# Performance work log

Hardware: AMD Instinct MI355X
Metric: run time of the kernel (lower is better)

Reference implementation:

```python
import jax, jax.numpy as jnp
import numpy as np
import math

B, S, D_IN, D_ATTN, D_HID = 4, 2048, 1024, 1024, 1024

def gelu_erf(x):
    return 0.5 * x * (1.0 + jax.lax.erf(x / math.sqrt(2.0)))

def setup_inputs() -> dict:
    key = jax.random.key(0)
    k = jax.random.split(key, 8)
    inputs = jax.random.normal(k[0], (B, S, D_IN), dtype=jnp.float32)
    attn_mask = jax.random.randint(k[1], (B, S, S), 0, 2, dtype=jnp.int32)
    sq = 1.0 / math.sqrt(D_IN)
    Wq = jax.random.normal(k[2], (D_IN, D_ATTN), dtype=jnp.float32) * sq
    bq = jnp.zeros((D_ATTN,), dtype=jnp.float32)
    Wk = jax.random.normal(k[3], (D_IN, D_ATTN), dtype=jnp.float32) * sq
    bk = jnp.zeros((D_ATTN,), dtype=jnp.float32)
    Wv = jax.random.normal(k[4], (D_IN, D_HID), dtype=jnp.float32) * sq
    bv = jnp.zeros((D_HID,), dtype=jnp.float32)
    return {"inputs": inputs, "attn_mask": attn_mask,
            "Wq": Wq, "bq": bq, "Wk": Wk, "bk": bk, "Wv": Wv, "bv": bv}

def reference(inputs, attn_mask, Wq, bq, Wk, bk, Wv, bv):
    # Q, K: [B, S, d_k]
    Q = inputs @ Wq + bq
    K = inputs @ Wk + bk
    scores = jnp.einsum('bqd,bkd->bqk', Q, K) / math.sqrt(D_ATTN)
    scores = scores + attn_mask.astype(scores.dtype) * (-1e9)
    attn = jax.nn.softmax(scores, axis=-1)
    WV = gelu_erf(inputs @ Wv + bv)           # [B, S, hidden]
    context = jnp.einsum('bqk,bkh->bqh', attn, WV)
    return (context, attn)
```

## Files before the change

kernel.cpp:

```cpp
#include <hip/hip_runtime.h>
#include <hip/hip_bf16.h>
#include <math.h>

#define B_   4
#define S_   2048
#define DIN  1024
#define DATT 1024
#define DHID 1024

typedef short bf16x8 __attribute__((ext_vector_type(8)));
typedef float f32x4  __attribute__((ext_vector_type(4)));

__device__ inline unsigned short f2bf(float f) {
    unsigned u = __float_as_uint(f);
    u += 0x7fffu + ((u >> 16) & 1u);
    return (unsigned short)(u >> 16);
}
__device__ inline float bf2f(unsigned u16) {
    return __uint_as_float(u16 << 16);
}
__device__ inline void gld16(const void* g, void* l) {
    __builtin_amdgcn_global_load_lds(
        (const __attribute__((address_space(1))) unsigned int*)g,
        (__attribute__((address_space(3))) unsigned int*)l, 16, 0, 0);
}
__device__ inline void xswz(int& bx, int& by, int& bz)
{
    int gx = gridDim.x, gy = gridDim.y, gz = gridDim.z;
    int nwg = gx * gy * gz;
    int lin = blockIdx.x + gx * (blockIdx.y + gy * blockIdx.z);
    int swz = (nwg & 7) ? lin : ((lin & 7) * (nwg >> 3) + (lin >> 3));
    bx = swz % gx;
    int t = swz / gx;
    by = t % gy;
    bz = t / gy;
}

__global__ __launch_bounds__(256)
void xcvt_k(const float* __restrict__ x, unsigned short* __restrict__ xb)
{
    int i = blockIdx.x * 256 + threadIdx.x;
    const float4* p = (const float4*)x + (size_t)i * 2;
    float4 v0 = p[0], v1 = p[1];
    uint4 o;
    o.x = (unsigned)f2bf(v0.x) | ((unsigned)f2bf(v0.y) << 16);
    o.y = (unsigned)f2bf(v0.z) | ((unsigned)f2bf(v0.w) << 16);
    o.z = (unsigned)f2bf(v1.x) | ((unsigned)f2bf(v1.y) << 16);
    o.w = (unsigned)f2bf(v1.z) | ((unsigned)f2bf(v1.w) << 16);
    ((uint4*)xb)[i] = o;
}

__global__ __launch_bounds__(256)
void wcvt_k(const float* __restrict__ Wq, const float* __restrict__ Wk,
            const float* __restrict__ Wv, unsigned short* __restrict__ Wt)
{
    int w = blockIdx.y;
    const float* W = (w == 0) ? Wq : ((w == 1) ? Wk : Wv);
    unsigned short* D = Wt + (size_t)w * DIN * DATT;
    int t = blockIdx.x * 256 + threadIdx.x;
    int n  = t >> 6;
    int kc = (t & 63) * 16;
    unsigned short r[16];
#pragma unroll
    for (int i = 0; i < 16; ++i) r[i] = f2bf(W[(size_t)(kc + i) * DATT + n]);
    uint4 o0, o1;
    o0.x = (unsigned)r[0] | ((unsigned)r[1] << 16);  o0.y = (unsigned)r[2] | ((unsigned)r[3] << 16);
    o0.z = (unsigned)r[4] | ((unsigned)r[5] << 16);  o0.w = (unsigned)r[6] | ((unsigned)r[7] << 16);
    o1.x = (unsigned)r[8] | ((unsigned)r[9] << 16);  o1.y = (unsigned)r[10] | ((unsigned)r[11] << 16);
    o1.z = (unsigned)r[12] | ((unsigned)r[13] << 16); o1.w = (unsigned)r[14] | ((unsigned)r[15] << 16);
    *(uint4*)(D + (size_t)n * DIN + kc)     = o0;
    *(uint4*)(D + (size_t)n * DIN + kc + 8) = o1;
}

__global__ __launch_bounds__(256)
void mpack_k(const int* __restrict__ m, unsigned* __restrict__ mb)
{
    int w = blockIdx.x * 256 + threadIdx.x;
    const uint4* p = (const uint4*)(m + (size_t)w * 32);
    unsigned bits = 0;
#pragma unroll
    for (int g = 0; g < 8; ++g) {
        uint4 v = p[g];
        bits |= (v.x ? 1u : 0u) << (g * 4 + 0);
        bits |= (v.y ? 1u : 0u) << (g * 4 + 1);
        bits |= (v.z ? 1u : 0u) << (g * 4 + 2);
        bits |= (v.w ? 1u : 0u) << (g * 4 + 3);
    }
    mb[w] = bits;
}

template<int EPI>
__global__ __launch_bounds__(512, 4)
void gemmS_k(const unsigned short* __restrict__ Ap, const unsigned short* __restrict__ Bp,
             const float* __restrict__ b0, const float* __restrict__ b1,
             const float* __restrict__ b2, const unsigned* __restrict__ mbits,
             void* __restrict__ Cp, void* __restrict__ Cp2,
             int K, int lda, int ldb, int ldc,
             long aStride, long bStride, long cStride, float scale)
{
    __shared__ __align__(16) unsigned short Al[256][64];
    __shared__ __align__(16) unsigned short Bl[128][64];

    int bx, by, z;
    xswz(bx, by, z);
    const int tid  = threadIdx.x;
    const int row0 = by * 256;
    const int col0 = bx * 128;
    const int wid  = tid >> 6, lane = tid & 63;
    const int lr = lane & 15, lg = lane >> 4;
    const int wm = wid >> 1, wn = wid & 1;
    const int wb = (tid & 448) * 16;

    const unsigned short* Ab = Ap + (size_t)aStride * z;
    const unsigned short* Bb = Bp + (size_t)bStride * z;

    f32x4 acc[4][4] = {};
    const int nt = K >> 6;

    const int srow = tid >> 3, sj = tid & 7;

    for (int t = 0; t < nt; ++t) {
        const int k0 = t << 6;
#pragma unroll
        for (int r = 0; r < 4; ++r) {
            int row = r * 64 + srow;
            gld16(Ab + (size_t)(row0 + row) * lda + k0 + ((sj ^ (row & 7)) << 3),
                  (char*)&Al[0][0] + r * 8192 + wb);
        }
#pragma unroll
        for (int r = 0; r < 2; ++r) {
            int row = r * 64 + srow;
            gld16(Bb + (size_t)(col0 + row) * ldb + k0 + ((sj ^ (row & 7)) << 3),
                  (char*)&Bl[0][0] + r * 8192 + wb);
        }
        __syncthreads();
#pragma unroll
        for (int s = 0; s < 2; ++s) {
            bf16x8 av[4], bv[4];
#pragma unroll
            for (int i = 0; i < 4; ++i) {
                int ra = wm * 64 + i * 16 + lr;
                av[i] = *(const bf16x8*)((const char*)&Al[0][0] + ra * 128 + ((((s << 2) | lg) ^ (ra & 7)) << 4));
                int rb = wn * 64 + i * 16 + lr;
                bv[i] = *(const bf16x8*)((const char*)&Bl[0][0] + rb * 128 + ((((s << 2) | lg) ^ (rb & 7)) << 4));
            }
#pragma unroll
            for (int mi = 0; mi < 4; ++mi)
#pragma unroll
                for (int ni = 0; ni < 4; ++ni)
                    acc[mi][ni] = __builtin_amdgcn_mfma_f32_16x16x32_bf16(av[mi], bv[ni], acc[mi][ni], 0, 0, 0);
        }
        __syncthreads();
    }

    if (EPI == 6) {
        int w = col0 >> 10;
        int cb0 = (col0 & 1023) + wn * 64;
        if (w < 2) {
            unsigned short* C = (unsigned short*)Cp + (size_t)w * ((size_t)B_ * S_ * DATT);
            const float* bias = w ? b1 : b0;
#pragma unroll
            for (int ni = 0; ni < 4; ++ni) {
                int col = cb0 + ni * 16 + lr;
                float bb = bias[col];
#pragma unroll
                for (int mi = 0; mi < 4; ++mi) {
                    int rowb = row0 + wm * 64 + mi * 16 + lg * 4;
#pragma unroll
                    for (int v = 0; v < 4; ++v)
                        C[(size_t)(rowb + v) * DATT + col] = f2bf(acc[mi][ni][v] + bb);
                }
            }
        } else {
            unsigned short* C = (unsigned short*)Cp2;
            int zz = row0 >> 11;
            int sb = (row0 & 2047) + wm * 64;
#pragma unroll
            for (int ni = 0; ni < 4; ++ni) {
                int col = cb0 + ni * 16 + lr;
                float bb = b2[col];
#pragma unroll
                for (int mi = 0; mi < 4; ++mi) {
                    unsigned short r[4];
#pragma unroll
                    for (int v = 0; v < 4; ++v) {
                        float xv = acc[mi][ni][v] + bb;
                        xv = 0.5f * xv * (1.0f + erff(xv * 0.70710678118654752f));
                        r[v] = f2bf(xv);
                    }
                    uint2 o;
                    o.x = (unsigned)r[0] | ((unsigned)r[1] << 16);
                    o.y = (unsigned)r[2] | ((unsigned)r[3] << 16);
                    *(uint2*)(C + ((size_t)zz * DHID + col) * S_ + sb + mi * 16 + lg * 4) = o;
                }
            }
        }
    } else {
        unsigned short* C = (unsigned short*)Cp + (size_t)cStride * z;
        const unsigned* mb = mbits + (size_t)z * (S_ * S_ / 32);
        const int wbase = (col0 + wn * 64) >> 5;
#pragma unroll
        for (int mi = 0; mi < 4; ++mi) {
            int rowb = row0 + wm * 64 + mi * 16 + lg * 4;
#pragma unroll
            for (int v = 0; v < 4; ++v) {
                int row = rowb + v;
                unsigned w0 = mb[(size_t)row * (S_ / 32) + wbase];
                unsigned w1 = mb[(size_t)row * (S_ / 32) + wbase + 1];
#pragma unroll
                for (int ni = 0; ni < 4; ++ni) {
                    int col = col0 + wn * 64 + ni * 16 + lr;
                    unsigned wsel = (ni & 2) ? w1 : w0;
                    float ev = ((wsel >> ((ni & 1) * 16 + lr)) & 1)
                             ? 0.0f : __expf(acc[mi][ni][v] * scale);
                    C[(size_t)row * ldc + col] = f2bf(ev);
                }
            }
        }
    }
}

template<int AMODE, int EPI>
__global__ __launch_bounds__(256)
void gemm_k(const void* __restrict__ Ap, const unsigned short* __restrict__ Bp,
            const float* __restrict__ b0, const float* __restrict__ b1,
            const float* __restrict__ b2, const int* __restrict__ maskp,
            void* __restrict__ Cp, void* __restrict__ Cp2,
            int K, int lda, int ldb, int ldc,
            long aStride, long bStride, long cStride, long mStride, float scale)
{
    __shared__ __align__(16) unsigned short sh[2][2][128][64];
    int bx, by, z;
    xswz(bx, by, z);
    const int tid  = threadIdx.x;
    const int row0 = by * 128;
    const int col0 = bx * 128;
    const int wave = tid >> 6, lane = tid & 63;
    const int lr = lane & 15, lg = lane >> 4;
    const int wm = (wave >> 1) * 64, wn = (wave & 1) * 64;
    const unsigned short* Bb = Bp + (size_t)bStride * z;
    f32x4 acc[4][4] = {};
    const int nt = K >> 6;
    auto stage = [&](int b, int k0) {
        if (AMODE == 0) {
            const unsigned short* A = (const unsigned short*)Ap + (size_t)aStride * z;
#pragma unroll
            for (int q = 0; q < 4; ++q) {
                int c = q * 256 + tid;
                int row = c >> 3, j = c & 7;
                gld16((const char*)(A + (size_t)(row0 + row) * lda + k0) + ((j ^ (row & 7)) << 4),
                      (char*)&sh[b][0][0][0] + ((q * 256 + (tid & 192)) << 4));
            }
        } else {
            const float* A = (const float*)Ap + (size_t)aStride * z;
#pragma unroll
            for (int q = 0; q < 4; ++q) {
                int c = q * 256 + tid;
                int row = c >> 3, j = c & 7;
                const float* src = A + (size_t)(row0 + row) * lda + k0 + ((j ^ (row & 7)) << 3);
                float4 v0 = *(const float4*)src;
                float4 v1 = *(const float4*)(src + 4);
                uint4 p;
                p.x = (unsigned)f2bf(v0.x) | ((unsigned)f2bf(v0.y) << 16);
                p.y = (unsigned)f2bf(v0.z) | ((unsigned)f2bf(v0.w) << 16);
                p.z = (unsigned)f2bf(v1.x) | ((unsigned)f2bf(v1.y) << 16);
                p.w = (unsigned)f2bf(v1.z) | ((unsigned)f2bf(v1.w) << 16);
                *(uint4*)((char*)&sh[b][0][0][0] + ((size_t)c << 4)) = p;
            }
        }
#pragma unroll
        for (int q = 0; q < 4; ++q) {
            int c = q * 256 + tid;
            int row = c >> 3, j = c & 7;
            gld16((const char*)(Bb + (size_t)(col0 + row) * ldb + k0) + ((j ^ (row & 7)) << 4),
                  (char*)&sh[b][1][0][0] + ((q * 256 + (tid & 192)) << 4));
        }
    };
    stage(0, 0);
    __syncthreads();
    int cur = 0;
    for (int t = 0; t < nt; ++t) {
        if (t + 1 < nt) stage(cur ^ 1, (t + 1) << 6);
        const char* baseA = (const char*)&sh[cur][0][0][0];
        const char* baseB = (const char*)&sh[cur][1][0][0];
        bf16x8 af[2][4], bfv[2][4];
#pragma unroll
        for (int s = 0; s < 2; ++s)
#pragma unroll
            for (int i = 0; i < 4; ++i) {
                int ra = wm + i * 16 + lr;
                af[s][i]  = *(const bf16x8*)(baseA + ra * 128 + ((((s << 2) | lg) ^ (ra & 7)) << 4));
                int rb = wn + i * 16 + lr;
                bfv[s][i] = *(const bf16x8*)(baseB + rb * 128 + ((((s << 2) | lg) ^ (rb & 7)) << 4));
            }
#pragma unroll
        for (int s = 0; s < 2; ++s)
#pragma unroll
            for (int mi = 0; mi < 4; ++mi)
#pragma unroll
                for (int ni = 0; ni < 4; ++ni)
                    acc[mi][ni] = __builtin_amdgcn_mfma_f32_16x16x32_bf16(af[s][mi], bfv[s][ni], acc[mi][ni], 0, 0, 0);
        if (t + 1 < nt) __syncthreads();
        cur ^= 1;
    }
    if (EPI == 6) {
        int w = col0 >> 10;
        int cb = (col0 & 1023) + wn;
        if (w < 2) {
            unsigned short* C = (unsigned short*)Cp + (size_t)w * ((size_t)B_ * S_ * DATT);
            const float* bias = w ? b1 : b0;
#pragma unroll
            for (int mi = 0; mi < 4; ++mi)
#pragma unroll
                for (int ni = 0; ni < 4; ++ni) {
                    int col = cb + ni * 16 + lr;
                    float bb = bias[col];
                    int rowb = row0 + wm + mi * 16 + lg * 4;
#pragma unroll
                    for (int v = 0; v < 4; ++v)
                        C[(size_t)(rowb + v) * DATT + col] = f2bf(acc[mi][ni][v] + bb);
                }
        } else {
            unsigned short* C = (unsigned short*)Cp2;
            int zz = row0 >> 11;
            int sb = (row0 & 2047) + wm;
#pragma unroll
            for (int mi = 0; mi < 4; ++mi)
#pragma unroll
                for (int ni = 0; ni < 4; ++ni) {
                    int col = cb + ni * 16 + lr;
                    float bb = b2[col];
                    unsigned short r[4];
#pragma unroll
                    for (int v = 0; v < 4; ++v) {
                        float xv = acc[mi][ni][v] + bb;
                        xv = 0.5f * xv * (1.0f + erff(xv * 0.70710678118654752f));
                        r[v] = f2bf(xv);
                    }
                    uint2 o;
                    o.x = (unsigned)r[0] | ((unsigned)r[1] << 16);
                    o.y = (unsigned)r[2] | ((unsigned)r[3] << 16);
                    *(uint2*)(C + ((size_t)zz * DHID + col) * S_ + sb + mi * 16 + lg * 4) = o;
                }
        }
    } else if (EPI == 5) {
        float* C = (float*)Cp + (size_t)cStride * z;
        const float* invs = b0 + (size_t)z * S_;
#pragma unroll
        for (int mi = 0; mi < 4; ++mi)
#pragma unroll
            for (int ni = 0; ni < 4; ++ni) {
                int col = col0 + wn + ni * 16 + lr;
                int rowb = row0 + wm + mi * 16 + lg * 4;
#pragma unroll
                for (int v = 0; v < 4; ++v)
                    C[(size_t)(rowb + v) * ldc + col] = acc[mi][ni][v] * invs[rowb + v];
            }
    } else {
        float* C = (float*)Cp + (size_t)cStride * z;
        const int* mp = (EPI == 2) ? (maskp + (size_t)mStride * z) : nullptr;
#pragma unroll
        for (int mi = 0; mi < 4; ++mi)
#pragma unroll
            for (int ni = 0; ni < 4; ++ni) {
                int col = col0 + wn + ni * 16 + lr;
                int rowb = row0 + wm + mi * 16 + lg * 4;
#pragma unroll
                for (int v = 0; v < 4; ++v) {
                    float val = acc[mi][ni][v];
                    if (EPI == 2) val = val * scale + (float)mp[(size_t)(rowb + v) * ldc + col] * (-1e9f);
                    C[(size_t)(rowb + v) * ldc + col] = val;
                }
            }
    }
}

__global__ __launch_bounds__(256)
void rownormM_k(const unsigned short* __restrict__ e, float* __restrict__ attn,
                float* __restrict__ invs)
{
    const int row = blockIdx.x;
    const int tid = threadIdx.x;
    uint4 u = ((const uint4*)(e + (size_t)row * S_))[tid];
    float f[8];
    f[0] = bf2f(u.x & 0xffffu); f[1] = bf2f(u.x >> 16);
    f[2] = bf2f(u.y & 0xffffu); f[3] = bf2f(u.y >> 16);
    f[4] = bf2f(u.z & 0xffffu); f[5] = bf2f(u.z >> 16);
    f[6] = bf2f(u.w & 0xffffu); f[7] = bf2f(u.w >> 16);
    float s = ((f[0] + f[1]) + (f[2] + f[3])) + ((f[4] + f[5]) + (f[6] + f[7]));
#pragma unroll
    for (int o = 32; o; o >>= 1) s += __shfl_xor(s, o);
    __shared__ float red[4];
    if ((tid & 63) == 0) red[tid >> 6] = s;
    __syncthreads();
    s = (red[0] + red[1]) + (red[2] + red[3]);
    float inv = 1.0f / s;
    float* p = attn + (size_t)row * S_;
    ((float4*)p)[tid * 2]     = make_float4(f[0] * inv, f[1] * inv, f[2] * inv, f[3] * inv);
    ((float4*)p)[tid * 2 + 1] = make_float4(f[4] * inv, f[5] * inv, f[6] * inv, f[7] * inv);
    if (tid == 0) invs[row] = inv;
}

template<bool WRITEATTN>
__global__ __launch_bounds__(256)
void rownorm_k(const unsigned short* __restrict__ e, float* __restrict__ attn,
               float* __restrict__ invs)
{
    const int row = blockIdx.x;
    const int tid = threadIdx.x;
    uint4 u = ((const uint4*)(e + (size_t)row * S_))[tid];
    float f[8];
    f[0] = bf2f(u.x & 0xffffu); f[1] = bf2f(u.x >> 16);
    f[2] = bf2f(u.y & 0xffffu); f[3] = bf2f(u.y >> 16);
    f[4] = bf2f(u.z & 0xffffu); f[5] = bf2f(u.z >> 16);
    f[6] = bf2f(u.w & 0xffffu); f[7] = bf2f(u.w >> 16);
    float s = ((f[0] + f[1]) + (f[2] + f[3])) + ((f[4] + f[5]) + (f[6] + f[7]));
#pragma unroll
    for (int o = 32; o; o >>= 1) s += __shfl_xor(s, o);
    __shared__ float red[4];
    if ((tid & 63) == 0) red[tid >> 6] = s;
    __syncthreads();
    s = (red[0] + red[1]) + (red[2] + red[3]);
    float inv = 1.0f / s;
    if (WRITEATTN) {
        float* p = attn + (size_t)row * S_;
        ((float4*)p)[tid * 2]     = make_float4(f[0] * inv, f[1] * inv, f[2] * inv, f[3] * inv);
        ((float4*)p)[tid * 2 + 1] = make_float4(f[4] * inv, f[5] * inv, f[6] * inv, f[7] * inv);
    } else {
        if (tid == 0) invs[row] = inv;
    }
}

__global__ __launch_bounds__(256)
void softmax_k(float* __restrict__ attn)
{
    const int row = blockIdx.x;
    float* p = attn + (size_t)row * S_;
    const int tid = threadIdx.x;
    float4 a = ((const float4*)p)[tid * 2];
    float4 b = ((const float4*)p)[tid * 2 + 1];
    float m = fmaxf(fmaxf(fmaxf(a.x, a.y), fmaxf(a.z, a.w)),
                    fmaxf(fmaxf(b.x, b.y), fmaxf(b.z, b.w)));
#pragma unroll
    for (int o = 32; o; o >>= 1) m = fmaxf(m, __shfl_xor(m, o));
    __shared__ float redm[4];
    __shared__ float reds[4];
    if ((tid & 63) == 0) redm[tid >> 6] = m;
    __syncthreads();
    m = fmaxf(fmaxf(redm[0], redm[1]), fmaxf(redm[2], redm[3]));
    float e[8];
    e[0] = expf(a.x - m); e[1] = expf(a.y - m); e[2] = expf(a.z - m); e[3] = expf(a.w - m);
    e[4] = expf(b.x - m); e[5] = expf(b.y - m); e[6] = expf(b.z - m); e[7] = expf(b.w - m);
    float s = e[0] + e[1] + e[2] + e[3] + e[4] + e[5] + e[6] + e[7];
#pragma unroll
    for (int o = 32; o; o >>= 1) s += __shfl_xor(s, o);
    if ((tid & 63) == 0) reds[tid >> 6] = s;
    __syncthreads();
    s = reds[0] + reds[1] + reds[2] + reds[3];
    float inv = 1.0f / s;
    ((float4*)p)[tid * 2]     = make_float4(e[0] * inv, e[1] * inv, e[2] * inv, e[3] * inv);
    ((float4*)p)[tid * 2 + 1] = make_float4(e[4] * inv, e[5] * inv, e[6] * inv, e[7] * inv);
}

extern "C" void kernel_launch(void* const* d_in, const int* in_sizes, int n_in,
                              void* d_out, int out_size, void* d_ws, size_t ws_size,
                              hipStream_t stream)
{
    const float* x    = (const float*)d_in[0];
    const int*   mask = (const int*)d_in[1];
    const float* Wq   = (const float*)d_in[2];
    const float* bq   = (const float*)d_in[3];
    const float* Wk   = (const float*)d_in[4];
    const float* bk   = (const float*)d_in[5];
    const float* Wv   = (const float*)d_in[6];
    const float* bv   = (const float*)d_in[7];

    float* ctx  = (float*)d_out;
    float* attn = ctx + (size_t)B_ * S_ * DHID;

    unsigned short* Qb = (unsigned short*)ctx;
    unsigned short* Kb = Qb + (size_t)B_ * S_ * DATT;
    unsigned short* Xb = (unsigned short*)attn;
    unsigned short* Wb = Xb + (size_t)B_ * S_ * DIN;

    const size_t eElems  = (size_t)B_ * S_ * S_;
    const size_t mWords  = eElems / 32;
    const size_t wvElems = (size_t)B_ * DHID * S_;

    size_t needFast = eElems * 2 + (size_t)B_ * S_ * 4 + mWords * 4 + wvElems * 2 + 256;
    size_t needMid  = eElems * 2 + (size_t)B_ * S_ * 4 + mWords * 4 + 256;

    dim3 blk(256), blk5(512);

    xcvt_k<<<dim3(4096), blk, 0, stream>>>(x, Xb);
    wcvt_k<<<dim3(256, 3), blk, 0, stream>>>(Wq, Wk, Wv, Wb);

    if (ws_size >= needFast) {
        unsigned short* e    = (unsigned short*)d_ws;
        float*          invs = (float*)(e + eElems);
        unsigned*       mb   = (unsigned*)(invs + (size_t)B_ * S_);
        unsigned short* WVbT = (unsigned short*)(mb + mWords);

        mpack_k<<<dim3(mWords / 256), blk, 0, stream>>>(mask, mb);
        gemmS_k<6><<<dim3(24, 32, 1), blk5, 0, stream>>>(
            Xb, Wb, bq, bk, bv, nullptr, Qb, WVbT,
            DIN, DIN, DIN, 0, 0, 0, 0, 1.0f);
        gemmS_k<4><<<dim3(16, 8, 4), blk5, 0, stream>>>(
            Qb, Kb, nullptr, nullptr, nullptr, mb, e, nullptr,
            DATT, DATT, DATT, S_,
            (long)S_ * DATT, (long)S_ * DATT, (long)S_ * S_, 0.03125f);
        rownormM_k<<<dim3(B_ * S_), blk, 0, stream>>>(e, attn, invs);
        gemm_k<0, 5><<<dim3(8, 16, 4), blk, 0, stream>>>(
            e, WVbT, invs, nullptr, nullptr, nullptr, ctx, nullptr,
            S_, S_, S_, DHID,
            (long)S_ * S_, (long)DHID * S_, (long)S_ * DHID, 0, 1.0f);
    } else if (ws_size >= needMid) {
        unsigned short* e    = (unsigned short*)d_ws;
        float*          invs = (float*)(e + eElems);
        unsigned*       mb   = (unsigned*)(invs + (size_t)B_ * S_);
        unsigned short* WVbT = Wb + (size_t)3 * DIN * DATT;

        mpack_k<<<dim3(mWords / 256), blk, 0, stream>>>(mask, mb);
        gemmS_k<6><<<dim3(24, 32, 1), blk5, 0, stream>>>(
            Xb, Wb, bq, bk, bv, nullptr, Qb, WVbT,
            DIN, DIN, DIN, 0, 0, 0, 0, 1.0f);
        gemmS_k<4><<<dim3(16, 8, 4), blk5, 0, stream>>>(
            Qb, Kb, nullptr, nullptr, nullptr, mb, e, nullptr,
            DATT, DATT, DATT, S_,
            (long)S_ * DATT, (long)S_ * DATT, (long)S_ * S_, 0.03125f);
        rownorm_k<false><<<dim3(B_ * S_), blk, 0, stream>>>(e, nullptr, invs);
        gemm_k<0, 5><<<dim3(8, 16, 4), blk, 0, stream>>>(
            e, WVbT, invs, nullptr, nullptr, nullptr, ctx, nullptr,
            S_, S_, S_, DHID,
            (long)S_ * S_, (long)DHID * S_, (long)S_ * DHID, 0, 1.0f);
        rownorm_k<true><<<dim3(B_ * S_), blk, 0, stream>>>(e, attn, nullptr);
    } else {
        unsigned short* WVw = (unsigned short*)d_ws;
        gemm_k<0, 6><<<dim3(24, 64, 1), blk, 0, stream>>>(
            Xb, Wb, bq, bk, bv, nullptr, Qb, WVw,
            DIN, DIN, DIN, 0, 0, 0, 0, 0, 1.0f);
        gemm_k<0, 2><<<dim3(16, 16, 4), blk, 0, stream>>>(
            Qb, Kb, nullptr, nullptr, nullptr, mask, attn, nullptr,
            DATT, DATT, DATT, S_,
            (long)S_ * DATT, (long)S_ * DATT, (long)S_ * S_, (long)S_ * S_, 0.03125f);
        softmax_k<<<dim3(B_ * S_), blk, 0, stream>>>(attn);
        gemm_k<1, 3><<<dim3(8, 16, 4), blk, 0, stream>>>(
            attn, WVw, nullptr, nullptr, nullptr, nullptr, ctx, nullptr,
            S_, S_, S_, DHID,
            (long)S_ * S_, (long)DHID * S_, (long)S_ * DHID, 0, 1.0f);
    }
}
```

Measured before the change: 215.3 us.

## Stage GEMM epilogues through swizzled LDS, merge prep kernels, and tile block mapping

Merges the three preprocessing kernels (input convert, weight convert/transpose, mask bit-pack) into one launch to cut launch overhead. Changes the GEMM epilogues to write each warp's output tile into swizzled shared memory first, then issue 16-byte coalesced global stores instead of scattered 2-byte or 8-byte writes. Also remaps workgroup indices into 4x2 tiles so neighbouring blocks share A/B panels in cache. Costs some extra LDS traffic and wait instructions in the epilogue.

```diff
diff --git a/kernel.cpp b/kernel.cpp
--- a/kernel.cpp
+++ b/kernel.cpp
@@ -24,69 +24,79 @@
         (const __attribute__((address_space(1))) unsigned int*)g,
         (__attribute__((address_space(3))) unsigned int*)l, 16, 0, 0);
 }
-__device__ inline void xswz(int& bx, int& by, int& bz)
-{
-    int gx = gridDim.x, gy = gridDim.y, gz = gridDim.z;
-    int nwg = gx * gy * gz;
+
+__device__ inline void xmap(int& bx, int& by, int& z)
+{
+    int gx = gridDim.x, gy = gridDim.y;
+    int nwg = gx * gy * gridDim.z;
     int lin = blockIdx.x + gx * (blockIdx.y + gy * blockIdx.z);
-    int swz = (nwg & 7) ? lin : ((lin & 7) * (nwg >> 3) + (lin >> 3));
-    bx = swz % gx;
-    int t = swz / gx;
-    by = t % gy;
-    bz = t / gy;
+    int s = (nwg & 7) ? lin : ((lin & 7) * (nwg >> 3) + (lin >> 3));
+    if (!(gx & 3) && !(gy & 1)) {
+        int cpz = (gx >> 2) * (gy >> 1);
+        int chunk = s >> 3, w = s & 7;
+        int cz = chunk / cpz, c2 = chunk % cpz;
+        int cx = c2 % (gx >> 2), cy = c2 / (gx >> 2);
+        bx = cx * 4 + (w & 3);
+        by = cy * 2 + (w >> 2);
+        z  = cz;
+    } else {
+        bx = s % gx;
+        int t = s / gx;
+        by = t % gy;
+        z  = t / gy;
+    }
 }
 
 __global__ __launch_bounds__(256)
-void xcvt_k(const float* __restrict__ x, unsigned short* __restrict__ xb)
-{
-    int i = blockIdx.x * 256 + threadIdx.x;
-    const float4* p = (const float4*)x + (size_t)i * 2;
-    float4 v0 = p[0], v1 = p[1];
-    uint4 o;
-    o.x = (unsigned)f2bf(v0.x) | ((unsigned)f2bf(v0.y) << 16);
-    o.y = (unsigned)f2bf(v0.z) | ((unsigned)f2bf(v0.w) << 16);
-    o.z = (unsigned)f2bf(v1.x) | ((unsigned)f2bf(v1.y) << 16);
-    o.w = (unsigned)f2bf(v1.z) | ((unsigned)f2bf(v1.w) << 16);
-    ((uint4*)xb)[i] = o;
-}
-
-__global__ __launch_bounds__(256)
-void wcvt_k(const float* __restrict__ Wq, const float* __restrict__ Wk,
-            const float* __restrict__ Wv, unsigned short* __restrict__ Wt)
-{
-    int w = blockIdx.y;
-    const float* W = (w == 0) ? Wq : ((w == 1) ? Wk : Wv);
-    unsigned short* D = Wt + (size_t)w * DIN * DATT;
-    int t = blockIdx.x * 256 + threadIdx.x;
-    int n  = t >> 6;
-    int kc = (t & 63) * 16;
-    unsigned short r[16];
-#pragma unroll
-    for (int i = 0; i < 16; ++i) r[i] = f2bf(W[(size_t)(kc + i) * DATT + n]);
-    uint4 o0, o1;
-    o0.x = (unsigned)r[0] | ((unsigned)r[1] << 16);  o0.y = (unsigned)r[2] | ((unsigned)r[3] << 16);
-    o0.z = (unsigned)r[4] | ((unsigned)r[5] << 16);  o0.w = (unsigned)r[6] | ((unsigned)r[7] << 16);
-    o1.x = (unsigned)r[8] | ((unsigned)r[9] << 16);  o1.y = (unsigned)r[10] | ((unsigned)r[11] << 16);
-    o1.z = (unsigned)r[12] | ((unsigned)r[13] << 16); o1.w = (unsigned)r[14] | ((unsigned)r[15] << 16);
-    *(uint4*)(D + (size_t)n * DIN + kc)     = o0;
-    *(uint4*)(D + (size_t)n * DIN + kc + 8) = o1;
-}
-
-__global__ __launch_bounds__(256)
-void mpack_k(const int* __restrict__ m, unsigned* __restrict__ mb)
-{
-    int w = blockIdx.x * 256 + threadIdx.x;
-    const uint4* p = (const uint4*)(m + (size_t)w * 32);
-    unsigned bits = 0;
-#pragma unroll
-    for (int g = 0; g < 8; ++g) {
-        uint4 v = p[g];
-        bits |= (v.x ? 1u : 0u) << (g * 4 + 0);
-        bits |= (v.y ? 1u : 0u) << (g * 4 + 1);
-        bits |= (v.z ? 1u : 0u) << (g * 4 + 2);
-        bits |= (v.w ? 1u : 0u) << (g * 4 + 3);
-    }
-    mb[w] = bits;
+void prep_k(const float* __restrict__ x, unsigned short* __restrict__ xb,
+            const float* __restrict__ Wq, const float* __restrict__ Wk,
+            const float* __restrict__ Wv, unsigned short* __restrict__ Wt,
+            const int* __restrict__ m, unsigned* __restrict__ mb)
+{
+    const int b = blockIdx.x;
+    const int tid = threadIdx.x;
+    if (b < 4096) {
+        int i = b * 256 + tid;
+        const float4* p = (const float4*)x + (size_t)i * 2;
+        float4 v0 = p[0], v1 = p[1];
+        uint4 o;
+        o.x = (unsigned)f2bf(v0.x) | ((unsigned)f2bf(v0.y) << 16);
+        o.y = (unsigned)f2bf(v0.z) | ((unsigned)f2bf(v0.w) << 16);
+        o.z = (unsigned)f2bf(v1.x) | ((unsigned)f2bf(v1.y) << 16);
+        o.w = (unsigned)f2bf(v1.z) | ((unsigned)f2bf(v1.w) << 16);
+        ((uint4*)xb)[i] = o;
+    } else if (b < 4864) {
+        int idx = b - 4096;
+        int w = idx >> 8;
+        const float* W = (w == 0) ? Wq : ((w == 1) ? Wk : Wv);
+        unsigned short* D = Wt + (size_t)w * DIN * DATT;
+        int t = (idx & 255) * 256 + tid;
+        int n  = t >> 6;
+        int kc = (t & 63) * 16;
+        unsigned short r[16];
+#pragma unroll
+        for (int i = 0; i < 16; ++i) r[i] = f2bf(W[(size_t)(kc + i) * DATT + n]);
+        uint4 o0, o1;
+        o0.x = (unsigned)r[0] | ((unsigned)r[1] << 16);  o0.y = (unsigned)r[2] | ((unsigned)r[3] << 16);
+        o0.z = (unsigned)r[4] | ((unsigned)r[5] << 16);  o0.w = (unsigned)r[6] | ((unsigned)r[7] << 16);
+        o1.x = (unsigned)r[8] | ((unsigned)r[9] << 16);  o1.y = (unsigned)r[10] | ((unsigned)r[11] << 16);
+        o1.z = (unsigned)r[12] | ((unsigned)r[13] << 16); o1.w = (unsigned)r[14] | ((unsigned)r[15] << 16);
+        *(uint4*)(D + (size_t)n * DIN + kc)     = o0;
+        *(uint4*)(D + (size_t)n * DIN + kc + 8) = o1;
+    } else {
+        int w = (b - 4864) * 256 + tid;
+        const uint4* p = (const uint4*)(m + (size_t)w * 32);
+        unsigned bits = 0;
+#pragma unroll
+        for (int g = 0; g < 8; ++g) {
+            uint4 v = p[g];
+            bits |= (v.x ? 1u : 0u) << (g * 4 + 0);
+            bits |= (v.y ? 1u : 0u) << (g * 4 + 1);
+            bits |= (v.z ? 1u : 0u) << (g * 4 + 2);
+            bits |= (v.w ? 1u : 0u) << (g * 4 + 3);
+        }
+        mb[w] = bits;
+    }
 }
 
 template<int EPI>
@@ -102,7 +112,7 @@
     __shared__ __align__(16) unsigned short Bl[128][64];
 
     int bx, by, z;
-    xswz(bx, by, z);
+    xmap(bx, by, z);
     const int tid  = threadIdx.x;
     const int row0 = by * 256;
     const int col0 = bx * 128;
@@ -153,46 +163,74 @@
         __syncthreads();
     }
 
+    unsigned short* scr = &Al[0][0] + wid * 2048;
+
     if (EPI == 6) {
         int w = col0 >> 10;
-        int cb0 = (col0 & 1023) + wn * 64;
         if (w < 2) {
             unsigned short* C = (unsigned short*)Cp + (size_t)w * ((size_t)B_ * S_ * DATT);
             const float* bias = w ? b1 : b0;
-#pragma unroll
-            for (int ni = 0; ni < 4; ++ni) {
-                int col = cb0 + ni * 16 + lr;
-                float bb = bias[col];
-#pragma unroll
-                for (int mi = 0; mi < 4; ++mi) {
-                    int rowb = row0 + wm * 64 + mi * 16 + lg * 4;
-#pragma unroll
-                    for (int v = 0; v < 4; ++v)
-                        C[(size_t)(rowb + v) * DATT + col] = f2bf(acc[mi][ni][v] + bb);
-                }
+            int cb0 = (col0 & 1023) + wn * 64;
+#pragma unroll
+            for (int h = 0; h < 2; ++h) {
+#pragma unroll
+                for (int mm = 0; mm < 2; ++mm) {
+                    int mi = h * 2 + mm;
+#pragma unroll
+                    for (int ni = 0; ni < 4; ++ni) {
+                        int lcol = ni * 16 + lr;
+                        float bb = bias[cb0 + lcol];
+#pragma unroll
+                        for (int v = 0; v < 4; ++v) {
+                            int wrow = mm * 16 + lg * 4 + v;
+                            scr[wrow * 64 + (((lcol >> 3) ^ (wrow & 7)) << 3) + (lcol & 7)] =
+                                f2bf(acc[mi][ni][v] + bb);
+                        }
+                    }
+                }
+                asm volatile("s_waitcnt lgkmcnt(0)" ::: "memory");
+#pragma unroll
+                for (int rr = 0; rr < 4; ++rr) {
+                    int lrow = rr * 8 + (lane >> 3);
+                    int chunk = lane & 7;
+                    uint4 u = *(const uint4*)&scr[lrow * 64 + ((chunk ^ (lrow & 7)) << 3)];
+                    int grow = row0 + wm * 64 + h * 32 + lrow;
+                    *(uint4*)(C + (size_t)grow * DATT + cb0 + chunk * 8) = u;
+                }
+                asm volatile("s_waitcnt lgkmcnt(0)" ::: "memory");
             }
         } else {
             unsigned short* C = (unsigned short*)Cp2;
             int zz = row0 >> 11;
-            int sb = (row0 & 2047) + wm * 64;
-#pragma unroll
-            for (int ni = 0; ni < 4; ++ni) {
-                int col = cb0 + ni * 16 + lr;
-                float bb = b2[col];
-#pragma unroll
-                for (int mi = 0; mi < 4; ++mi) {
-                    unsigned short r[4];
-#pragma unroll
-                    for (int v = 0; v < 4; ++v) {
-                        float xv = acc[mi][ni][v] + bb;
-                        xv = 0.5f * xv * (1.0f + erff(xv * 0.70710678118654752f));
-                        r[v] = f2bf(xv);
-                    }
-                    uint2 o;
-                    o.x = (unsigned)r[0] | ((unsigned)r[1] << 16);
-                    o.y = (unsigned)r[2] | ((unsigned)r[3] << 16);
-                    *(uint2*)(C + ((size_t)zz * DHID + col) * S_ + sb + mi * 16 + lg * 4) = o;
-                }
+            int sb0 = (row0 & 2047) + wm * 64;
+            int hb0 = (col0 & 1023) + wn * 64;
+#pragma unroll
+            for (int h = 0; h < 2; ++h) {
+#pragma unroll
+                for (int nn = 0; nn < 2; ++nn) {
+                    int ni = h * 2 + nn;
+                    int lcol = nn * 16 + lr;
+                    float bb = b2[hb0 + h * 32 + lcol];
+#pragma unroll
+                    for (int mi = 0; mi < 4; ++mi)
+#pragma unroll
+                        for (int v = 0; v < 4; ++v) {
+                            int lrow = mi * 16 + lg * 4 + v;
+                            float xv = acc[mi][ni][v] + bb;
+                            xv = 0.5f * xv * (1.0f + erff(xv * 0.70710678118654752f));
+                            scr[lcol * 64 + (((lrow >> 3) ^ (lcol & 7)) << 3) + (lrow & 7)] = f2bf(xv);
+                        }
+                }
+                asm volatile("s_waitcnt lgkmcnt(0)" ::: "memory");
+#pragma unroll
+                for (int rr = 0; rr < 4; ++rr) {
+                    int lhid = rr * 8 + (lane >> 3);
+                    int chunk = lane & 7;
+                    uint4 u = *(const uint4*)&scr[lhid * 64 + ((chunk ^ (lhid & 7)) << 3)];
+                    int ghid = hb0 + h * 32 + lhid;
+                    *(uint4*)(C + ((size_t)zz * DHID + ghid) * S_ + sb0 + chunk * 8) = u;
+                }
+                asm volatile("s_waitcnt lgkmcnt(0)" ::: "memory");
             }
         }
     } else {
@@ -200,22 +238,36 @@
         const unsigned* mb = mbits + (size_t)z * (S_ * S_ / 32);
         const int wbase = (col0 + wn * 64) >> 5;
 #pragma unroll
-        for (int mi = 0; mi < 4; ++mi) {
-            int rowb = row0 + wm * 64 + mi * 16 + lg * 4;
-#pragma unroll
-            for (int v = 0; v < 4; ++v) {
-                int row = rowb + v;
-                unsigned w0 = mb[(size_t)row * (S_ / 32) + wbase];
-                unsigned w1 = mb[(size_t)row * (S_ / 32) + wbase + 1];
-#pragma unroll
-                for (int ni = 0; ni < 4; ++ni) {
-                    int col = col0 + wn * 64 + ni * 16 + lr;
-                    unsigned wsel = (ni & 2) ? w1 : w0;
-                    float ev = ((wsel >> ((ni & 1) * 16 + lr)) & 1)
-                             ? 0.0f : __expf(acc[mi][ni][v] * scale);
-                    C[(size_t)row * ldc + col] = f2bf(ev);
-                }
-            }
+        for (int h = 0; h < 2; ++h) {
+#pragma unroll
+            for (int mm = 0; mm < 2; ++mm) {
+                int mi = h * 2 + mm;
+#pragma unroll
+                for (int v = 0; v < 4; ++v) {
+                    int row = row0 + wm * 64 + mi * 16 + lg * 4 + v;
+                    unsigned w0 = mb[(size_t)row * (S_ / 32) + wbase];
+                    unsigned w1 = mb[(size_t)row * (S_ / 32) + wbase + 1];
+                    int wrow = mm * 16 + lg * 4 + v;
+#pragma unroll
+                    for (int ni = 0; ni < 4; ++ni) {
+                        int lcol = ni * 16 + lr;
+                        unsigned wsel = (ni & 2) ? w1 : w0;
+                        float ev = ((wsel >> ((ni & 1) * 16 + lr)) & 1)
+                                 ? 0.0f : __expf(acc[mi][ni][v] * scale);
+                        scr[wrow * 64 + (((lcol >> 3) ^ (wrow & 7)) << 3) + (lcol & 7)] = f2bf(ev);
+                    }
+                }
+            }
+            asm volatile("s_waitcnt lgkmcnt(0)" ::: "memory");
+#pragma unroll
+            for (int rr = 0; rr < 4; ++rr) {
+                int lrow = rr * 8 + (lane >> 3);
+                int chunk = lane & 7;
+                uint4 u = *(const uint4*)&scr[lrow * 64 + ((chunk ^ (lrow & 7)) << 3)];
+                int grow = row0 + wm * 64 + h * 32 + lrow;
+                *(uint4*)(C + (size_t)grow * ldc + col0 + wn * 64 + chunk * 8) = u;
+            }
+            asm volatile("s_waitcnt lgkmcnt(0)" ::: "memory");
         }
     }
 }
@@ -231,7 +283,7 @@
 {
     __shared__ __align__(16) unsigned short sh[2][2][128][64];
     int bx, by, z;
-    xswz(bx, by, z);
+    xmap(bx, by, z);
     const int tid  = threadIdx.x;
     const int row0 = by * 128;
     const int col0 = bx * 128;
@@ -492,16 +544,13 @@
 
     dim3 blk(256), blk5(512);
 
-    xcvt_k<<<dim3(4096), blk, 0, stream>>>(x, Xb);
-    wcvt_k<<<dim3(256, 3), blk, 0, stream>>>(Wq, Wk, Wv, Wb);
-
     if (ws_size >= needFast) {
         unsigned short* e    = (unsigned short*)d_ws;
         float*          invs = (float*)(e + eElems);
         unsigned*       mb   = (unsigned*)(invs + (size_t)B_ * S_);
         unsigned short* WVbT = (unsigned short*)(mb + mWords);
 
-        mpack_k<<<dim3(mWords / 256), blk, 0, stream>>>(mask, mb);
+        prep_k<<<dim3(6912), blk, 0, stream>>>(x, Xb, Wq, Wk, Wv, Wb, mask, mb);
         gemmS_k<6><<<dim3(24, 32, 1), blk5, 0, stream>>>(
             Xb, Wb, bq, bk, bv, nullptr, Qb, WVbT,
             DIN, DIN, DIN, 0, 0, 0, 0, 1.0f);
@@ -520,7 +569,7 @@
         unsigned*       mb   = (unsigned*)(invs + (size_t)B_ * S_);
         unsigned short* WVbT = Wb + (size_t)3 * DIN * DATT;
 
-        mpack_k<<<dim3(mWords / 256), blk, 0, stream>>>(mask, mb);
+        prep_k<<<dim3(6912), blk, 0, stream>>>(x, Xb, Wq, Wk, Wv, Wb, mask, mb);
         gemmS_k<6><<<dim3(24, 32, 1), blk5, 0, stream>>>(
             Xb, Wb, bq, bk, bv, nullptr, Qb, WVbT,
             DIN, DIN, DIN, 0, 0, 0, 0, 1.0f);
@@ -536,6 +585,7 @@
         rownorm_k<true><<<dim3(B_ * S_), blk, 0, stream>>>(e, attn, nullptr);
     } else {
         unsigned short* WVw = (unsigned short*)d_ws;
+        prep_k<<<dim3(4864), blk, 0, stream>>>(x, Xb, Wq, Wk, Wv, Wb, mask, nullptr);
         gemm_k<0, 6><<<dim3(24, 64, 1), blk, 0, stream>>>(
             Xb, Wb, bq, bk, bv, nullptr, Qb, WVw,
             DIN, DIN, DIN, 0, 0, 0, 0, 0, 1.0f);
```

Result: faster. 210.9 us (median of 4 runs) (-2.1%).
